# Performance work log

Hardware: AMD Instinct MI355X
Metric: run time of the kernel (lower is better)

Reference implementation:

```python
import jax, jax.numpy as jnp
import numpy as np

D = 1024  # 2 * hidden_size

def setup_inputs() -> dict:
    key = jax.random.key(0)
    ks = jax.random.split(key, 7)
    s = 1.0 / np.sqrt(D)
    return {
        "lstm_output": jax.random.normal(ks[0], (8, 2048, D), dtype=jnp.float32),
        "Wq": jax.random.uniform(ks[1], (D, D), jnp.float32, -s, s),
        "bq": jax.random.uniform(ks[2], (D,), jnp.float32, -s, s),
        "Wk": jax.random.uniform(ks[3], (D, D), jnp.float32, -s, s),
        "bk": jax.random.uniform(ks[4], (D,), jnp.float32, -s, s),
        "Wv": jax.random.uniform(ks[5], (D, D), jnp.float32, -s, s),
        "bv": jax.random.uniform(ks[6], (D,), jnp.float32, -s, s),
    }

def reference(lstm_output, Wq, bq, Wk, bk, Wv, bv):
    # x: [B, S, D]
    Q = lstm_output @ Wq + bq
    K = lstm_output @ Wk + bk
    V = lstm_output @ Wv + bv
    # Unscaled attention scores: [B, S, S]
    scores = jnp.einsum("bqd,bkd->bqk", Q, K)
    weights = jax.nn.softmax(scores, axis=-1)
    context = jnp.einsum("bqk,bkd->bqd", weights, V)
    return context
```

## Files before the change

### kernel.cpp

```cpp
#include <hip/hip_runtime.h>

typedef _Float16 half8 __attribute__((ext_vector_type(8)));
typedef _Float16 half4 __attribute__((ext_vector_type(4)));
typedef short short8 __attribute__((ext_vector_type(8)));
typedef unsigned short ushort4v __attribute__((ext_vector_type(4)));
typedef float floatx4 __attribute__((ext_vector_type(4)));

#define ASYNC16(g, l) __builtin_amdgcn_global_load_lds( \
    (const __attribute__((address_space(1))) void*)(g),  \
    (__attribute__((address_space(3))) void*)(l), 16, 0, 0)

__device__ inline unsigned short f2bf(float f) {
    unsigned u = __builtin_bit_cast(unsigned, f);
    u += 0x7fff + ((u >> 16) & 1);
    return (unsigned short)(u >> 16);
}
__device__ inline float bf2f(unsigned short b) {
    unsigned u = (unsigned)b << 16;
    return __builtin_bit_cast(float, u);
}

__global__ void cvt_f2h(const float* __restrict__ in, _Float16* __restrict__ out, int n4)
{
    int i = blockIdx.x * blockDim.x + threadIdx.x;
    const int stride = gridDim.x * blockDim.x;
    for (; i < n4; i += stride) {
        float4 v = ((const float4*)in)[i];
        half4 h = { (_Float16)v.x, (_Float16)v.y, (_Float16)v.z, (_Float16)v.w };
        ((half4*)out)[i] = h;
    }
}

__global__ void transpose_w(const float* __restrict__ Wq, const float* __restrict__ Wk,
                            const float* __restrict__ Wv, _Float16* __restrict__ Wt)
{
    const float* W = (blockIdx.z == 0) ? Wq : (blockIdx.z == 1) ? Wk : Wv;
    _Float16* out = Wt + (size_t)blockIdx.z * 1024 * 1024;
    __shared__ float t[32][33];
    const int tx = threadIdx.x, ty = threadIdx.y;
    const int k0 = blockIdx.x * 32, n0 = blockIdx.y * 32;
#pragma unroll
    for (int i = 0; i < 32; i += 8)
        t[ty + i][tx] = W[(size_t)(k0 + ty + i) * 1024 + n0 + tx];
    __syncthreads();
#pragma unroll
    for (int i = 0; i < 32; i += 8)
        out[(size_t)(n0 + ty + i) * 1024 + k0 + tx] = (_Float16)t[tx][ty + i];
}

template<bool BF16>
__device__ __forceinline__ floatx4 MF(short8 a, short8 b, floatx4 c) {
    if constexpr (BF16)
        return __builtin_amdgcn_mfma_f32_16x16x32_bf16(a, b, c, 0, 0, 0);
    else
        return __builtin_amdgcn_mfma_f32_16x16x32_f16(
            __builtin_bit_cast(half8, a), __builtin_bit_cast(half8, b), c, 0, 0, 0);
}

template<int LDA, int LDB, int NT, bool BF16>
__device__ __forceinline__ void gemm_core8(
    const unsigned short* __restrict__ Ab, const unsigned short* __restrict__ Bb,
    unsigned short* sA, unsigned short* sB, floatx4 (&acc)[8][4])
{
    const int tid = threadIdx.x;
    const int lane = tid & 63, quad = lane >> 4, l15 = lane & 15;
    const int wave = tid >> 6;
    const int wm = wave >> 2, wn = wave & 3;
    const int rowbase = wm * 128, colbase = wn * 64;
    const int sw = l15 & 7;

    long srcA[2], srcB[2];
    int dst[2];
#pragma unroll
    for (int u = 0; u < 2; ++u) {
        const int c = tid + u * 512;
        const int row = c >> 3;
        const int g = (c & 7) ^ (row & 7);
        srcA[u] = (long)row * LDA + g * 8;
        srcB[u] = (long)row * LDB + g * 8;
        dst[u] = c * 16;
    }

    const char* aRd[2];
    const char* bRd[2];
#pragma unroll
    for (int kk = 0; kk < 2; ++kk) {
        const int ck = ((kk * 4 + quad) ^ sw) * 16;
        aRd[kk] = (const char*)sA + (rowbase + l15) * 128 + ck;
        bRd[kk] = (const char*)sB + (colbase + l15) * 128 + ck;
    }

    short8 a[4][2], b[2][2][2];

    auto stgA = [&](int p, int h, int kt) {
#pragma unroll
        for (int u = 0; u < 2; ++u)
            ASYNC16(Ab + (long)kt * 64 + (long)h * (128 * LDA) + srcA[u],
                    (char*)sA + p * 32768 + h * 16384 + dst[u]);
    };
    auto stgB = [&](int p, int h, int kt) {
#pragma unroll
        for (int u = 0; u < 2; ++u)
            ASYNC16(Bb + (long)kt * 64 + (long)h * (128 * LDB) + srcB[u],
                    (char*)sB + p * 32768 + h * 16384 + dst[u]);
    };
    auto rdA = [&](int mq, int p) {
#pragma unroll
        for (int ii = 0; ii < 4; ++ii)
#pragma unroll
            for (int kk = 0; kk < 2; ++kk)
                a[ii][kk] = *(const short8*)(aRd[kk] + p * 32768 + mq * 8192 + ii * 2048);
    };
    auto rdB = [&](int nq, int p) {
#pragma unroll
        for (int jj = 0; jj < 2; ++jj)
#pragma unroll
            for (int kk = 0; kk < 2; ++kk)
                b[nq][jj][kk] = *(const short8*)(bRd[kk] + p * 32768 + nq * 4096 + jj * 2048);
    };
    auto mm = [&](int mq, int nq) {
#pragma unroll
        for (int ii = 0; ii < 4; ++ii)
#pragma unroll
            for (int jj = 0; jj < 2; ++jj)
#pragma unroll
                for (int kk = 0; kk < 2; ++kk)
                    acc[mq * 4 + ii][nq * 2 + jj] =
                        MF<BF16>(a[ii][kk], b[nq][jj][kk], acc[mq * 4 + ii][nq * 2 + jj]);
    };
    auto bar   = [] { __builtin_amdgcn_s_barrier(); };
    auto lgkm0 = [] { asm volatile("s_waitcnt lgkmcnt(0)" ::: "memory"); };
    auto vm4   = [] { asm volatile("s_waitcnt vmcnt(4)" ::: "memory"); };
    auto pr1   = [] { __builtin_amdgcn_s_setprio(1); };
    auto pr0   = [] { __builtin_amdgcn_s_setprio(0); };

    stgA(0, 0, 0); stgA(0, 1, 0); stgB(0, 0, 0); stgB(0, 1, 0);
    stgB(1, 0, 1); stgB(1, 1, 1);
    vm4();
    bar();
    rdA(0, 0); rdB(0, 0);

#pragma unroll 1
    for (int i = 0; i < NT / 2; ++i) {
        const int t1 = 2 * i + 1;
        const int t2 = (2 * i + 2) & (NT - 1);
        const int t3 = (2 * i + 3) & (NT - 1);
        stgA(1, 0, t1);
        bar(); lgkm0();
        pr1(); mm(0, 0); rdB(1, 0); pr0();
        bar();
        stgA(1, 1, t1);
        bar(); lgkm0();
        pr1(); mm(0, 1); rdA(1, 0); pr0();
        bar();
        stgB(0, 0, t2);
        bar(); lgkm0();
        pr1(); mm(1, 1); pr0();
        bar();
        stgB(0, 1, t2); vm4();
        bar();
        pr1(); mm(1, 0); rdA(0, 1); rdB(0, 1); pr0();
        bar();
        stgA(0, 0, t2);
        bar(); lgkm0();
        pr1(); mm(0, 0); rdB(1, 1); pr0();
        bar();
        stgA(0, 1, t2);
        bar(); lgkm0();
        pr1(); mm(0, 1); rdA(1, 1); pr0();
        bar();
        stgB(1, 0, t3);
        bar(); lgkm0();
        pr1(); mm(1, 1); pr0();
        bar();
        stgB(1, 1, t3); vm4();
        bar();
        pr1(); mm(1, 0); rdA(0, 0); rdB(0, 0); pr0();
        bar();
    }
    asm volatile("s_waitcnt vmcnt(0)" ::: "memory");
}

__global__ __launch_bounds__(512, 2)
void gemm_qkv8(const unsigned short* __restrict__ X, const unsigned short* __restrict__ Wt,
               const float* __restrict__ bq, const float* __restrict__ bk,
               const float* __restrict__ bv,
               _Float16* __restrict__ Qh, _Float16* __restrict__ Kh,
               unsigned short* __restrict__ Vt)
{
    extern __shared__ unsigned short smem[];
    unsigned short* sA = smem;
    unsigned short* sB = smem + 32768;

    constexpr int GX = 12, GY = 64, NWG = GX * GY;
    const int d = blockIdx.y * GX + blockIdx.x;
    const int wf = (d & 7) * (NWG >> 3) + (d >> 3);
    const int bx = wf % GX, by = wf / GX;

    const long m0 = (long)by * 256;
    const int n0 = bx * 256;

    floatx4 acc[8][4] = {};
    gemm_core8<1024, 1024, 16, false>(X + m0 * 1024, Wt + (long)n0 * 1024, sA, sB, acc);

    const int tid = threadIdx.x;
    const int lane = tid & 63, quad = lane >> 4, l15 = lane & 15;
    const int wave = tid >> 6, wm = wave >> 2, wn = wave & 3;

    const int which = n0 >> 10;
    const int ncol0 = n0 & 1023;
    const float* bias = (which == 0) ? bq : (which == 1) ? bk : bv;

    if (which < 2) {
        _Float16* O = which ? Kh : Qh;
#pragma unroll
        for (int i = 0; i < 8; ++i) {
            const long mb = m0 + wm * 128 + i * 16 + quad * 4;
#pragma unroll
            for (int j = 0; j < 4; ++j) {
                const int col = ncol0 + wn * 64 + j * 16 + l15;
                const float bb = bias[col];
                _Float16* op = O + mb * 1024 + col;
#pragma unroll
                for (int r = 0; r < 4; ++r)
                    op[(long)r * 1024] = (_Float16)(acc[i][j][r] + bb);
            }
        }
    } else {
#pragma unroll
        for (int i = 0; i < 8; ++i) {
            const long mb = m0 + wm * 128 + i * 16 + quad * 4;
            const int bz = (int)(mb >> 11);
            const int s = (int)(mb & 2047);
#pragma unroll
            for (int j = 0; j < 4; ++j) {
                const int col = ncol0 + wn * 64 + j * 16 + l15;
                const float bb = bias[col];
                ushort4v h;
#pragma unroll
                for (int r = 0; r < 4; ++r) h[r] = f2bf(acc[i][j][r] + bb);
                *(ushort4v*)(Vt + (long)bz * 2097152 + (long)col * 2048 + s) = h;
            }
        }
    }
}

__global__ __launch_bounds__(512, 2)
void gemm_sc8(const unsigned short* __restrict__ Q, const unsigned short* __restrict__ K,
              unsigned short* __restrict__ E, float* __restrict__ rowsum)
{
    extern __shared__ unsigned short smem[];
    unsigned short* sA = smem;
    unsigned short* sB = smem + 32768;

    constexpr int GX = 8, GY = 8, NWG = GX * GY;
    const int d = blockIdx.y * GX + blockIdx.x;
    const int wf = (d & 7) * (NWG >> 3) + (d >> 3);
    const int bx = wf % GX, by = wf / GX;

    const long m0 = (long)by * 256;
    const long n0 = (long)bx * 256;
    const long zo = (long)blockIdx.z * 2097152;
    unsigned short* Eb = E + (long)blockIdx.z * 4194304;
    float* rs = rowsum + (long)blockIdx.z * 2048;

    floatx4 acc[8][4] = {};
    gemm_core8<1024, 1024, 16, false>(Q + zo + m0 * 1024, K + zo + n0 * 1024, sA, sB, acc);

    const int tid = threadIdx.x;
    const int lane = tid & 63, quad = lane >> 4, l15 = lane & 15;
    const int wave = tid >> 6, wm = wave >> 2, wn = wave & 3;

#pragma unroll
    for (int i = 0; i < 8; ++i) {
        const int rowb = (int)m0 + wm * 128 + i * 16 + quad * 4;
#pragma unroll
        for (int r = 0; r < 4; ++r) {
            float sl = 0.f;
#pragma unroll
            for (int j = 0; j < 4; ++j) {
                const long col = n0 + wn * 64 + j * 16 + l15;
                const unsigned short bb = f2bf(__expf(acc[i][j][r] - 40.0f));
                Eb[(long)(rowb + r) * 2048 + col] = bb;
                sl += bf2f(bb);
            }
            sl += __shfl_xor(sl, 1);
            sl += __shfl_xor(sl, 2);
            sl += __shfl_xor(sl, 4);
            sl += __shfl_xor(sl, 8);
            if (l15 == 0) atomicAdd(&rs[rowb + r], sl);
        }
    }
}

__global__ __launch_bounds__(512, 2)
void gemm_pv8(const unsigned short* __restrict__ E, const unsigned short* __restrict__ Vt,
              const float* __restrict__ rowsum, float* __restrict__ C)
{
    extern __shared__ unsigned short smem[];
    unsigned short* sA = smem;
    unsigned short* sB = smem + 32768;

    constexpr int GX = 4, GY = 8, NWG = GX * GY;
    const int d = blockIdx.y * GX + blockIdx.x;
    const int wf = (d & 7) * (NWG >> 3) + (d >> 3);
    const int bx = wf % GX, by = wf / GX;

    const long m0 = (long)by * 256;
    const long n0 = (long)bx * 256;

    const unsigned short* Ab = E + (long)blockIdx.z * 4194304 + m0 * 2048;
    const unsigned short* Bb = Vt + (long)blockIdx.z * 2097152 + n0 * 2048;
    const float* rs = rowsum + (long)blockIdx.z * 2048;
    float* Cb = C + (long)blockIdx.z * 2097152;

    floatx4 acc[8][4] = {};
    gemm_core8<2048, 2048, 32, true>(Ab, Bb, sA, sB, acc);

    const int tid = threadIdx.x;
    const int lane = tid & 63, quad = lane >> 4, l15 = lane & 15;
    const int wave = tid >> 6, wm = wave >> 2, wn = wave & 3;

#pragma unroll
    for (int i = 0; i < 8; ++i) {
        const int rowb = (int)m0 + wm * 128 + i * 16 + quad * 4;
#pragma unroll
        for (int r = 0; r < 4; ++r) {
            const float inv = 1.0f / rs[rowb + r];
            float* cp = Cb + (long)(rowb + r) * 1024 + n0 + wn * 64 + l15;
#pragma unroll
            for (int j = 0; j < 4; ++j)
                cp[j * 16] = acc[i][j][r] * inv;
        }
    }
}

extern "C" void kernel_launch(void* const* d_in, const int* in_sizes, int n_in,
                              void* d_out, int out_size, void* d_ws, size_t ws_size,
                              hipStream_t stream)
{
    const float* x  = (const float*)d_in[0];
    const float* Wq = (const float*)d_in[1];
    const float* bq = (const float*)d_in[2];
    const float* Wk = (const float*)d_in[3];
    const float* bk = (const float*)d_in[4];
    const float* Wv = (const float*)d_in[5];
    const float* bv = (const float*)d_in[6];
    float* out = (float*)d_out;

    char* ws = (char*)d_ws;
    _Float16* Qh = (_Float16*)ws;
    _Float16* Kh = Qh + 16777216;
    unsigned short* Vt = (unsigned short*)(Kh + 16777216);
    char* region = ws + 100663296;
    _Float16* xh = (_Float16*)region;
    _Float16* Wt = xh + 16777216;
    unsigned short* E = (unsigned short*)region;

    int c = 8;
    size_t region_sz;
    for (;;) {
        region_sz = (size_t)c * 8388608ull;
        if (region_sz < 39845888ull) region_sz = 39845888ull;
        if (100663296ull + region_sz + 65536ull <= ws_size || c == 1) break;
        c >>= 1;
    }
    float* rowsum = (float*)(ws + 100663296 + region_sz);

    static bool attr_done = false;
    if (!attr_done) {
        hipFuncSetAttribute((const void*)gemm_qkv8,
                            hipFuncAttributeMaxDynamicSharedMemorySize, 131072);
        hipFuncSetAttribute((const void*)gemm_sc8,
                            hipFuncAttributeMaxDynamicSharedMemorySize, 131072);
        hipFuncSetAttribute((const void*)gemm_pv8,
                            hipFuncAttributeMaxDynamicSharedMemorySize, 131072);
        attr_done = true;
    }

    cvt_f2h<<<2048, 256, 0, stream>>>(x, xh, 16777216 / 4);
    transpose_w<<<dim3(32, 32, 3), dim3(32, 8, 1), 0, stream>>>(Wq, Wk, Wv, Wt);
    gemm_qkv8<<<dim3(12, 64, 1), 512, 131072, stream>>>(
        (const unsigned short*)xh, (const unsigned short*)Wt, bq, bk, bv, Qh, Kh, Vt);

    for (int b0 = 0; b0 < 8; b0 += c) {
        int cc = (8 - b0 < c) ? (8 - b0) : c;
        hipMemsetAsync(rowsum, 0, (size_t)cc * 2048 * 4, stream);
        gemm_sc8<<<dim3(8, 8, cc), 512, 131072, stream>>>(
            (const unsigned short*)(Qh + (long)b0 * 2097152),
            (const unsigned short*)(Kh + (long)b0 * 2097152), E, rowsum);
        gemm_pv8<<<dim3(4, 8, cc), 512, 131072, stream>>>(
            E, Vt + (long)b0 * 2097152, rowsum, out + (long)b0 * 2097152);
    }
}
```

Before: 384.7 us.

## Replace PV GEMM with smaller 128x128-tile kernel using static LDS

Swaps the 256x256-tile, 512-thread PV GEMM built on the shared pipelined core for a self-contained 128x128-tile, 256-thread kernel with a 32KB static LDS footprint and XOR-swizzled async global-to-LDS loads. The grid grows fourfold per batch chunk, which raises parallelism and occupancy for this small GEMM. In exchange there is less data reuse per tile and no double buffering, since each k-step syncs twice around a single LDS buffer and loads are not overlapped with MFMA work.

```diff
diff --git a/kernel.cpp b/kernel.cpp
--- a/kernel.cpp
+++ b/kernel.cpp
@@ -293,41 +293,69 @@
     }
 }
 
-__global__ __launch_bounds__(512, 2)
-void gemm_pv8(const unsigned short* __restrict__ E, const unsigned short* __restrict__ Vt,
-              const float* __restrict__ rowsum, float* __restrict__ C)
-{
-    extern __shared__ unsigned short smem[];
-    unsigned short* sA = smem;
-    unsigned short* sB = smem + 32768;
-
-    constexpr int GX = 4, GY = 8, NWG = GX * GY;
-    const int d = blockIdx.y * GX + blockIdx.x;
-    const int wf = (d & 7) * (NWG >> 3) + (d >> 3);
-    const int bx = wf % GX, by = wf / GX;
-
-    const long m0 = (long)by * 256;
-    const long n0 = (long)bx * 256;
+__global__ __launch_bounds__(256, 2)
+void gemm_pv(const unsigned short* __restrict__ E, const unsigned short* __restrict__ Vt,
+             const float* __restrict__ rowsum, float* __restrict__ C)
+{
+    __shared__ __align__(16) unsigned short sA[128 * 64];
+    __shared__ __align__(16) unsigned short sB[128 * 64];
+    const int tid = threadIdx.x;
+    const int lane = tid & 63, wave = tid >> 6;
+    const int quad = lane >> 4, l15 = lane & 15;
+    const int wm = (wave & 1) * 64, wn = (wave >> 1) * 64;
+    const long m0 = (long)blockIdx.y * 128;
+    const long n0 = (long)blockIdx.x * 128;
 
     const unsigned short* Ab = E + (long)blockIdx.z * 4194304 + m0 * 2048;
     const unsigned short* Bb = Vt + (long)blockIdx.z * 2097152 + n0 * 2048;
     const float* rs = rowsum + (long)blockIdx.z * 2048;
     float* Cb = C + (long)blockIdx.z * 2097152;
 
-    floatx4 acc[8][4] = {};
-    gemm_core8<2048, 2048, 32, true>(Ab, Bb, sA, sB, acc);
-
-    const int tid = threadIdx.x;
-    const int lane = tid & 63, quad = lane >> 4, l15 = lane & 15;
-    const int wave = tid >> 6, wm = wave >> 2, wn = wave & 3;
-
-#pragma unroll
-    for (int i = 0; i < 8; ++i) {
-        const int rowb = (int)m0 + wm * 128 + i * 16 + quad * 4;
+    long offA[4];
+    int ldsOff[4];
+#pragma unroll
+    for (int u = 0; u < 4; ++u) {
+        const int c = tid + u * 256;
+        const int row = c >> 3, g = (c & 7) ^ (row & 7);
+        offA[u] = (long)row * 2048 + g * 8;
+        ldsOff[u] = c * 16;
+    }
+    const int sw = l15 & 7;
+
+    floatx4 acc[4][4] = {};
+
+    for (int k0 = 0; k0 < 2048; k0 += 64) {
+        __syncthreads();
+#pragma unroll
+        for (int u = 0; u < 4; ++u) {
+            ASYNC16(Ab + offA[u] + k0, (char*)sA + ldsOff[u]);
+            ASYNC16(Bb + offA[u] + k0, (char*)sB + ldsOff[u]);
+        }
+        __syncthreads();
+#pragma unroll
+        for (int s = 0; s < 2; ++s) {
+            const int ck = ((s * 4 + quad) ^ sw) * 8;
+            short8 af[4], bf[4];
+#pragma unroll
+            for (int i = 0; i < 4; ++i) {
+                af[i] = *(const short8*)(sA + (wm + i * 16 + l15) * 64 + ck);
+                bf[i] = *(const short8*)(sB + (wn + i * 16 + l15) * 64 + ck);
+            }
+#pragma unroll
+            for (int i = 0; i < 4; ++i)
+#pragma unroll
+                for (int j = 0; j < 4; ++j)
+                    acc[i][j] = __builtin_amdgcn_mfma_f32_16x16x32_bf16(af[i], bf[j], acc[i][j], 0, 0, 0);
+        }
+    }
+
+#pragma unroll
+    for (int i = 0; i < 4; ++i) {
+        const int rowb = (int)(m0 + wm + i * 16 + quad * 4);
 #pragma unroll
         for (int r = 0; r < 4; ++r) {
             const float inv = 1.0f / rs[rowb + r];
-            float* cp = Cb + (long)(rowb + r) * 1024 + n0 + wn * 64 + l15;
+            float* cp = Cb + (long)(rowb + r) * 1024 + n0 + wn + l15;
 #pragma unroll
             for (int j = 0; j < 4; ++j)
                 cp[j * 16] = acc[i][j][r] * inv;
@@ -373,8 +401,6 @@
                             hipFuncAttributeMaxDynamicSharedMemorySize, 131072);
         hipFuncSetAttribute((const void*)gemm_sc8,
                             hipFuncAttributeMaxDynamicSharedMemorySize, 131072);
-        hipFuncSetAttribute((const void*)gemm_pv8,
-                            hipFuncAttributeMaxDynamicSharedMemorySize, 131072);
         attr_done = true;
     }
 
@@ -389,7 +415,7 @@
         gemm_sc8<<<dim3(8, 8, cc), 512, 131072, stream>>>(
             (const unsigned short*)(Qh + (long)b0 * 2097152),
             (const unsigned short*)(Kh + (long)b0 * 2097152), E, rowsum);
-        gemm_pv8<<<dim3(4, 8, cc), 512, 131072, stream>>>(
+        gemm_pv<<<dim3(8, 16, cc), 256, 0, stream>>>(
             E, Vt + (long)b0 * 2097152, rowsum, out + (long)b0 * 2097152);
     }
 }
```

Measured after the change: 409.1 us. +6.3%, slower.
